# Kernel optimization log

Measured on AMD Instinct MI355X. Metric: run time of the kernel, lower is better.

The kernel has to match this reference:

```python
import jax, jax.numpy as jnp
import numpy as np

N_NODES = 50000
N_EDGES = 1600000
NFEAT = 512
NHID = 64
H1 = 8      # nheads[0]
H2 = 1      # nheads[1]
NCLASS = 16
ALPHA = 0.2  # leaky_relu negative slope


def setup_inputs() -> dict:
    key = jax.random.key(0)
    ks = jax.random.split(key, 6)
    x = jax.random.normal(ks[0], (N_NODES, NFEAT), jnp.float32)
    edge_index = jax.random.randint(ks[1], (2, N_EDGES), 0, N_NODES, jnp.int32)

    def glorot(k, shape):
        fan_in, fan_out = shape[-2], shape[-1]
        std = (2.0 / (fan_in + fan_out)) ** 0.5
        return jax.random.normal(k, shape, jnp.float32) * std

    W1 = glorot(ks[2], (H1, NFEAT, NHID))
    a1 = jax.random.normal(ks[3], (H1, 2 * NHID), jnp.float32) * 0.1
    W2 = glorot(ks[4], (H2, NHID * H1, NCLASS))
    a2 = jax.random.normal(ks[5], (H2, 2 * NCLASS), jnp.float32) * 0.1
    return {"x": x, "edge_index": edge_index, "W1": W1, "a1": a1, "W2": W2, "a2": a2}


def _spgat_head(x, W, a, src, dst, n_nodes, apply_elu):
    # Sparse GAT head (pyGAT SpGraphAttentionLayer, eval mode / no dropout).
    h = x @ W                              # [N, F']
    f = W.shape[1]
    # a . [h_src || h_dst] decomposed into per-node scores (same math, no [E,2F'] concat)
    s_src = h @ a[:f]                      # [N]
    s_dst = h @ a[f:]                      # [N]
    logits = s_src[src] + s_dst[dst]       # [E]
    e = jnp.exp(-jax.nn.leaky_relu(logits, ALPHA))  # edge_e = exp(-leakyrelu(...)) > 0
    rowsum = jax.ops.segment_sum(e, src, num_segments=n_nodes)            # [N]
    agg = jax.ops.segment_sum(e[:, None] * h[dst], src, num_segments=n_nodes)  # [N, F']
    h_prime = agg / rowsum[:, None]
    return jax.nn.elu(h_prime) if apply_elu else h_prime


def reference(x, edge_index, W1, a1, W2, a2):
    src, dst = edge_index[0], edge_index[1]
    n = x.shape[0]
    # Layer 1: H1 heads, concat=True (elu inside each head), concatenated on features
    h = jnp.concatenate(
        [_spgat_head(x, W1[i], a1[i], src, dst, n, True) for i in range(W1.shape[0])],
        axis=1,
    )  # [N, H1*NHID]
    # Layer 2: H2 heads, concat=False, stacked then averaged
    outs = jnp.stack(
        [_spgat_head(h, W2[i], a2[i], src, dst, n, False) for i in range(W2.shape[0])],
        axis=2,
    )  # [N, NCLASS, H2]
    out = jnp.mean(outs, axis=2)
    return jax.nn.log_softmax(jax.nn.elu(out), axis=1)
```

## Files before the change

### kernel.cpp

```cpp
#include <hip/hip_runtime.h>

#define NN 50000
#define NE 1600000
#define NFEAT 512
#define NHID 64
#define H1 8
#define NCLASS 16
#define ALPHA 0.2f

#define BUCKETS 391
#define CAP 6144
#define EPB 4096
#define PASSA_BLKS 391
#define PASSB_BLKS 391
#define PACK_BLKS 1024
#define PACK2_BLKS 32
#define GEMMB 391
#define NROW_PAD 50048

typedef __attribute__((ext_vector_type(8))) short short8;
typedef __attribute__((ext_vector_type(4))) float floatx4;
typedef __attribute__((ext_vector_type(2))) float floatx2;
typedef __attribute__((ext_vector_type(2))) long longx2;

__device__ __forceinline__ float elu_f(float x) { return x > 0.0f ? x : __expf(x) - 1.0f; }
__device__ __forceinline__ float edge_w(float logit) {
    return __expf(-fmaxf(logit, ALPHA * logit));
}
__device__ __forceinline__ ushort f2bf(float f) {
    uint u = __float_as_uint(f);
    return (ushort)((u + 0x7FFFu + ((u >> 16) & 1)) >> 16);
}
__device__ __forceinline__ uint packbf2(float lo, float hi) {
    return (uint)f2bf(lo) | ((uint)f2bf(hi) << 16);
}
__device__ __forceinline__ float bf2f(ushort v) { return __uint_as_float((uint)v << 16); }
__device__ __forceinline__ unsigned char f2fp8(float v) {
    return (unsigned char)(__builtin_amdgcn_cvt_pk_fp8_f32(v, v, 0, false) & 0xFF);
}
__device__ __forceinline__ uint pack4fp8(float a, float b, float c, float d) {
    uint u = __builtin_amdgcn_cvt_pk_fp8_f32(a, b, 0, false);
    return __builtin_amdgcn_cvt_pk_fp8_f32(c, d, u, true);
}

#define GLD16(g, l)                                                              \
    __builtin_amdgcn_global_load_lds(                                            \
        (const __attribute__((address_space(1))) unsigned int*)(g),              \
        (__attribute__((address_space(3))) unsigned int*)(l), 16, 0, 0)

__device__ __forceinline__ int scan256x(int v, int tid, int* wsum, int* tot) {
    int s = v;
#pragma unroll
    for (int o = 1; o < 64; o <<= 1) {
        int u = __shfl_up(s, o);
        if ((tid & 63) >= o) s += u;
    }
    __syncthreads();
    if ((tid & 63) == 63) wsum[tid >> 6] = s;
    __syncthreads();
    int off = 0, t = 0;
#pragma unroll
    for (int i = 0; i < 4; i++) {
        int x = wsum[i];
        if (i < (tid >> 6)) off += x;
        t += x;
    }
    *tot = t;
    return s - v + off;
}

__device__ __forceinline__ int scan512x(int v, int tid, int* wsum, int* tot) {
    int s = v;
#pragma unroll
    for (int o = 1; o < 64; o <<= 1) {
        int u = __shfl_up(s, o);
        if ((tid & 63) >= o) s += u;
    }
    __syncthreads();
    if ((tid & 63) == 63) wsum[tid >> 6] = s;
    __syncthreads();
    int off = 0, t = 0;
#pragma unroll
    for (int i = 0; i < 8; i++) {
        int x = wsum[i];
        if (i < (tid >> 6)) off += x;
        t += x;
    }
    *tot = t;
    return s - v + off;
}

__global__ __launch_bounds__(256) void prep_k(const float* __restrict__ W1,
                                              unsigned char* __restrict__ Wt8,
                                              const float* __restrict__ W2,
                                              ushort* __restrict__ W2tb,
                                              const int* __restrict__ ei,
                                              int* __restrict__ bucket_cnt,
                                              uint* __restrict__ staging) {
    int b = blockIdx.x;
    if (b < PACK_BLKS) {
        int i = b * 256 + threadIdx.x;
        int c = i >> 9, o = i & 511;
        int c6 = o >> 6, qhi = (o >> 4) & 3, kb = (o >> 3) & 1, bb = o & 7;
        int quad = qhi ^ ((c >> 1) & 3);
        int k = c6 * 64 + kb * 32 + quad * 8 + bb;
        Wt8[i] = f2fp8(W1[((c >> 6) * 512 + k) * 64 + (c & 63)]);
        return;
    }
    if (b < PACK_BLKS + PACK2_BLKS) {
        int i = (b - PACK_BLKS) * 256 + threadIdx.x;
        int c = i >> 9, f = i & 511;
        W2tb[i] = f2bf(W2[f * 16 + c]);
        return;
    }
    __shared__ int histA[BUCKETS];
    __shared__ int exclA[BUCKETS];
    __shared__ int baseA[BUCKETS];
    __shared__ int wsumA[4];
    __shared__ uint ebuf[EPB];
    const int blk = b - PACK_BLKS - PACK2_BLKS;
    const int t = threadIdx.x;
    const int e0 = blk * EPB;
    const int cntb = min(EPB, NE - e0);
    for (int i = t; i < BUCKETS; i += 256) histA[i] = 0;
    __syncthreads();
    int br[16]; uint pay[16];
#pragma unroll
    for (int i = 0; i < 16; i++) {
        int e = e0 + i * 256 + t;
        br[i] = -1;
        if (e < NE) {
            int s = ei[e], d = ei[NE + e];
            int bu = s >> 7;
            pay[i] = ((uint)bu << 23) | ((uint)(s & 127) << 16) | (uint)d;
            br[i] = (bu << 12) | atomicAdd(&histA[bu], 1);
        }
    }
    __syncthreads();
    int tot0, tot1;
    int v0 = histA[t];
    int v1 = (t + 256 < BUCKETS) ? histA[t + 256] : 0;
    int p0 = scan256x(v0, t, wsumA, &tot0);
    int p1 = scan256x(v1, t, wsumA, &tot1);
    exclA[t] = p0;
    if (t + 256 < BUCKETS) exclA[t + 256] = p1 + tot0;
    __syncthreads();
    for (int i = t; i < BUCKETS; i += 256) {
        int c = histA[i];
        if (c > 0) baseA[i] = atomicAdd(&bucket_cnt[i], c);
    }
#pragma unroll
    for (int i = 0; i < 16; i++)
        if (br[i] >= 0) ebuf[exclA[br[i] >> 12] + (br[i] & 4095)] = pay[i];
    __syncthreads();
    for (int j = t; j < cntb; j += 256) {
        uint v = ebuf[j];
        int bu = v >> 23;
        int pos = baseA[bu] + (j - exclA[bu]);
        staging[(size_t)bu * CAP + pos] = v;
    }
}

__global__ __launch_bounds__(512) void passb_k(const int* __restrict__ bucket_cnt,
                                               const uint* __restrict__ staging,
                                               ushort* __restrict__ csru,
                                               int* __restrict__ rowptr) {
    __shared__ int hist2w[1024];
    __shared__ int cur2w[1024];
    __shared__ int wbase[1024];
    __shared__ int excl2[128];
    __shared__ int wsum2[8];
    __shared__ int sbs;
    const int tid = threadIdx.x;
    const int b = blockIdx.x;
    const int cnt = bucket_cnt[b];
    const uint* sg = staging + (size_t)b * CAP;
    const int wv = tid >> 6;
    for (int i = tid; i < 2048; i += 512) {
        if (i < 1024) hist2w[i] = 0; else cur2w[i - 1024] = 0;
    }
    if (tid < 64) {
        int c[7]; int s0 = 0;
#pragma unroll
        for (int i = 0; i < 7; i++) {
            int bi = tid * 7 + i;
            c[i] = (bi < BUCKETS) ? bucket_cnt[bi] : 0;
            s0 += c[i];
        }
        int sc = s0;
#pragma unroll
        for (int o = 1; o < 64; o <<= 1) {
            int u = __shfl_up(sc, o);
            if (tid >= o) sc += u;
        }
        int run = sc - s0;
        if (tid == b / 7) {
            int part = run;
            for (int i = 0; i < b % 7; i++) part += c[i];
            sbs = part;
        }
    }
    if (b == 0 && tid == 0) rowptr[NN] = NE;
    __syncthreads();
    const int sbase = sbs;
    for (int e = tid; e < cnt; e += 512)
        atomicAdd(&hist2w[wv * 128 + ((sg[e] >> 16) & 127)], 1);
    __syncthreads();
    int v = 0;
    if (tid < 128) {
        int run = 0;
#pragma unroll
        for (int w = 0; w < 8; w++) {
            wbase[w * 128 + tid] = run;
            run += hist2w[w * 128 + tid];
        }
        v = run;
    }
    int tot;
    int ex = scan512x(v, tid, wsum2, &tot);
    if (tid < 128) {
        excl2[tid] = ex;
        int n = b * 128 + tid;
        if (n < NN) rowptr[n] = sbase + ex;
    }
    __syncthreads();
    for (int e = tid; e < cnt; e += 512) {
        uint u = sg[e];
        int sl = (u >> 16) & 127;
        int pos = excl2[sl] + wbase[wv * 128 + sl] + atomicAdd(&cur2w[wv * 128 + sl], 1);
        csru[sbase + pos] = (ushort)(u & 0xFFFF);
    }
}

__global__ __launch_bounds__(512) void gemm1_k(const float* __restrict__ x,
                                               const unsigned char* __restrict__ Wt8,
                                               const float* __restrict__ a1,
                                               unsigned char* __restrict__ h8,
                                               float* __restrict__ s1s,
                                               float* __restrict__ s1d) {
    __shared__ unsigned char Bs[32768];
    const int tid = threadIdx.x;
    const int gb = blockIdx.x;
    const int row0 = gb * 128;
    const int wv = tid >> 6, lane = tid & 63;
    const int l16 = lane & 15, quad = lane >> 4;
    const int qoff = ((quad ^ ((l16 >> 1) & 3)) << 4);
    const int mA = wv * 16 + (lane >> 2);
    const int offA = (lane & 3) * 16;
    const unsigned char* gB0 = Wt8 + (size_t)(0 * 128 + mA) * 512 + offA;
    const unsigned char* gB1 = Wt8 + (size_t)(1 * 128 + mA) * 512 + offA;
    const unsigned char* gB2 = Wt8 + (size_t)(2 * 128 + mA) * 512 + offA;
    const unsigned char* gB3 = Wt8 + (size_t)(3 * 128 + mA) * 512 + offA;
    const int arow = row0 + wv * 16 + l16;
    const int arowc = min(arow, NN - 1);
    const float* xA = x + (size_t)arowc * 512 + quad * 8;

    floatx4 acc[32];
#pragma unroll
    for (int ct = 0; ct < 32; ct++) acc[ct] = (floatx4){0.f, 0.f, 0.f, 0.f};

    for (int t = 0; t < 8; t++) {
        const int k0 = t * 64;
        GLD16(gB0 + k0, Bs + wv * 1024);
        GLD16(gB1 + k0, Bs + 8192 + wv * 1024);
        GLD16(gB2 + k0, Bs + 16384 + wv * 1024);
        GLD16(gB3 + k0, Bs + 24576 + wv * 1024);
        float4 f0 = *(const float4*)(xA + k0);
        float4 f1 = *(const float4*)(xA + k0 + 4);
        float4 f2 = *(const float4*)(xA + k0 + 32);
        float4 f3 = *(const float4*)(xA + k0 + 36);
        uint u0 = pack4fp8(f0.x, f0.y, f0.z, f0.w);
        uint u1 = pack4fp8(f1.x, f1.y, f1.z, f1.w);
        uint u2 = pack4fp8(f2.x, f2.y, f2.z, f2.w);
        uint u3 = pack4fp8(f3.x, f3.y, f3.z, f3.w);
        long ax = (long)(((unsigned long)u1 << 32) | u0);
        long ay = (long)(((unsigned long)u3 << 32) | u2);
        __syncthreads();
        const unsigned char* bp = Bs + l16 * 64 + qoff;
#pragma unroll
        for (int ct = 0; ct < 32; ct++) {
            longx2 bv = *(const longx2*)(bp + ct * 1024);
            acc[ct] = __builtin_amdgcn_mfma_f32_16x16x32_fp8_fp8(ax, bv.x, acc[ct], 0, 0, 0);
            acc[ct] = __builtin_amdgcn_mfma_f32_16x16x32_fp8_fp8(ay, bv.y, acc[ct], 0, 0, 0);
        }
        __syncthreads();
    }

    const int rbase = row0 + wv * 16 + quad * 4;
#pragma unroll
    for (int hh = 0; hh < 8; hh++) {
        float ss[4] = {0.f, 0.f, 0.f, 0.f}, sd[4] = {0.f, 0.f, 0.f, 0.f};
#pragma unroll
        for (int c4 = 0; c4 < 4; c4++) {
            int ct = hh * 4 + c4;
            int colg = ct * 16 + l16;
            float avs = a1[hh * 128 + c4 * 16 + l16];
            float avd = a1[hh * 128 + 64 + c4 * 16 + l16];
#pragma unroll
            for (int r = 0; r < 4; r++) {
                float v = acc[ct][r];
                ss[r] += v * avs;
                sd[r] += v * avd;
                int row = rbase + r;
                if (row < NN) h8[(size_t)row * 512 + colg] = f2fp8(v);
            }
        }
#pragma unroll
        for (int r = 0; r < 4; r++) {
            float a_ = ss[r], b_ = sd[r];
#pragma unroll
            for (int o = 1; o < 16; o <<= 1) {
                a_ += __shfl_xor(a_, o);
                b_ += __shfl_xor(b_, o);
            }
            int row = rbase + r;
            if (l16 == 0 && row < NN) {
                s1s[row * 8 + hh] = a_;
                s1d[row * 8 + hh] = b_;
            }
        }
    }
}

__global__ __launch_bounds__(256) void agg1f_k(const int n_base,
                                               const int* __restrict__ rowptr,
                                               const ushort* __restrict__ csru,
                                               const float* __restrict__ s1s,
                                               const float* __restrict__ s1d,
                                               const uint2* __restrict__ hb8,
                                               const ushort* __restrict__ W2tb,
                                               const float* __restrict__ a2,
                                               ushort* __restrict__ h2b,
                                               float* __restrict__ s2s,
                                               float* __restrict__ s2d) {
    __shared__ ushort Ash[16 * 512];
    unsigned char* ashb = (unsigned char*)Ash;
    const int tid = threadIdx.x;
    const int wv = tid >> 6, lane = tid & 63;
    const int n0 = n_base + blockIdx.x * 4;
    const int n = n0 + wv;
    const int head8 = lane >> 3;
    const int hb = head8 << 3;
    const int esub = lane & 7;
    const int beg = rowptr[n];
    const int deg = rowptr[n + 1] - beg;
    const float ssrc = s1s[n * 8 + head8];
    floatx2 acc[4] = {};
    float rsum = 0.f;

    const int G = (deg + 7) >> 3;
    const int dm1 = deg - 1;
    if (G > 0) {
        int dA = csru[beg + min(esub, dm1)];
        float tw = s1d[dA * 8 + head8];
        for (int g = 0; g < G; g++) {
            uint2 v[8];
#pragma unroll
            for (int j = 0; j < 8; j++) {
                int dj = __shfl(dA, j);
                v[j] = hb8[(uint)dj * 64 + lane];
            }
            int dAn = csru[beg + min(g * 8 + 8 + esub, dm1)];
            float twn = s1d[dAn * 8 + head8];
            float w = (g * 8 + esub <= dm1) ? edge_w(ssrc + tw) : 0.f;
            rsum += w;
#pragma unroll
            for (int j = 0; j < 8; j++) {
                float wj = __shfl(w, hb + j);
                floatx2 w2 = (floatx2){wj, wj};
                acc[0] += w2 * __builtin_amdgcn_cvt_pk_f32_fp8(v[j].x, false);
                acc[1] += w2 * __builtin_amdgcn_cvt_pk_f32_fp8(v[j].x, true);
                acc[2] += w2 * __builtin_amdgcn_cvt_pk_f32_fp8(v[j].y, false);
                acc[3] += w2 * __builtin_amdgcn_cvt_pk_f32_fp8(v[j].y, true);
            }
            dA = dAn;
            tw = twn;
        }
    }

    rsum += __shfl_xor(rsum, 1);
    rsum += __shfl_xor(rsum, 2);
    rsum += __shfl_xor(rsum, 4);
    float inv = 1.0f / rsum;
    uint4 o;
    o.x = packbf2(elu_f(acc[0][0] * inv), elu_f(acc[0][1] * inv));
    o.y = packbf2(elu_f(acc[1][0] * inv), elu_f(acc[1][1] * inv));
    o.z = packbf2(elu_f(acc[2][0] * inv), elu_f(acc[2][1] * inv));
    o.w = packbf2(elu_f(acc[3][0] * inv), elu_f(acc[3][1] * inv));
    *(uint4*)(ashb + wv * 1024 + ((lane * 16) ^ (wv << 4))) = o;
    __syncthreads();

    if (wv == 0) {
        const int l16 = lane & 15, q = lane >> 4;
        floatx4 c2 = (floatx4){0.f, 0.f, 0.f, 0.f};
#pragma unroll
        for (int s = 0; s < 16; s++) {
            short8 af = *(const short8*)(ashb + l16 * 1024 +
                                         ((s * 64 + q * 16) ^ ((l16 & 7) << 4)));
            short8 bf = *(const short8*)(W2tb + l16 * 512 + s * 32 + q * 8);
            c2 = __builtin_amdgcn_mfma_f32_16x16x32_bf16(af, bf, c2, 0, 0, 0);
        }
        if (q == 0) {
#pragma unroll
            for (int r = 0; r < 4; r++) h2b[(size_t)(n0 + r) * 16 + l16] = f2bf(c2[r]);
        }
#pragma unroll
        for (int r = 0; r < 4; r++) {
            float ssv = c2[r] * a2[l16];
            float sdv = c2[r] * a2[16 + l16];
#pragma unroll
            for (int oo = 1; oo < 16; oo <<= 1) {
                ssv += __shfl_xor(ssv, oo);
                sdv += __shfl_xor(sdv, oo);
            }
            if (lane == 0) { s2s[n0 + r] = ssv; s2d[n0 + r] = sdv; }
        }
    }
}

__global__ __launch_bounds__(256) void agg2_k(const int* __restrict__ rowptr,
                                              const ushort* __restrict__ csru,
                                              const float* __restrict__ s2s,
                                              const float* __restrict__ s2d,
                                              const ushort* __restrict__ h2b,
                                              float* __restrict__ out) {
    const int n = (blockIdx.x * 256 + threadIdx.x) >> 6;
    const int lane = threadIdx.x & 63;
    if (n >= NN) return;
    const int beg = rowptr[n], end = rowptr[n + 1];
    const float sn = s2s[n];
    const int sub = lane >> 4, f = lane & 15;
    float acc = 0.f, rsum = 0.f;
    int e = beg + sub;
    for (; e + 12 < end; e += 16) {
        int d0 = csru[e], d1 = csru[e + 4], d2 = csru[e + 8], d3 = csru[e + 12];
        float t0 = s2d[d0], t1 = s2d[d1], t2 = s2d[d2], t3 = s2d[d3];
        float g0 = bf2f(h2b[(uint)d0 * 16 + f]), g1 = bf2f(h2b[(uint)d1 * 16 + f]);
        float g2 = bf2f(h2b[(uint)d2 * 16 + f]), g3 = bf2f(h2b[(uint)d3 * 16 + f]);
        float w0 = edge_w(sn + t0), w1 = edge_w(sn + t1);
        float w2 = edge_w(sn + t2), w3 = edge_w(sn + t3);
        acc += w0 * g0 + w1 * g1 + w2 * g2 + w3 * g3;
        rsum += w0 + w1 + w2 + w3;
    }
    for (; e < end; e += 4) {
        int d0 = csru[e];
        float w0 = edge_w(sn + s2d[d0]);
        acc += w0 * bf2f(h2b[(uint)d0 * 16 + f]);
        rsum += w0;
    }
    acc += __shfl_down(acc, 32);
    acc += __shfl_down(acc, 16);
    rsum += __shfl_down(rsum, 32);
    rsum += __shfl_down(rsum, 16);
    if (lane < 16) {
        float v = elu_f(acc / rsum);
        float m = v;
#pragma unroll
        for (int o = 8; o > 0; o >>= 1) m = fmaxf(m, __shfl_xor(m, o));
        float ex = __expf(v - m), s = ex;
#pragma unroll
        for (int o = 8; o > 0; o >>= 1) s += __shfl_xor(s, o);
        out[(size_t)n * 16 + f] = v - (__logf(s) + m);
    }
}

extern "C" void kernel_launch(void* const* d_in, const int* in_sizes, int n_in,
                              void* d_out, int out_size, void* d_ws, size_t ws_size,
                              hipStream_t stream) {
    const float* x  = (const float*)d_in[0];
    const int*   ei = (const int*)d_in[1];
    const float* W1 = (const float*)d_in[2];
    const float* a1 = (const float*)d_in[3];
    const float* W2 = (const float*)d_in[4];
    const float* a2 = (const float*)d_in[5];
    float* out = (float*)d_out;

    unsigned char* h8  = (unsigned char*)d_ws;
    unsigned char* Wt8 = h8 + (size_t)NROW_PAD * 512;
    ushort* W2tb  = (ushort*)(Wt8 + 512 * 512);
    float* s1s    = (float*)(W2tb + 8192);
    float* s1d    = s1s + (size_t)NN * H1;
    int* rowptr   = (int*)(s1d + (size_t)NN * H1);
    int* bucket_cnt   = rowptr + 50056;
    int* bucket_start = bucket_cnt + 512;
    ushort* csru  = (ushort*)(bucket_start + 512);
    ushort* h2b   = csru + NE;
    float* s2s    = (float*)(h2b + (size_t)NN * 16);
    float* s2d    = s2s + NN;
    uint* staging = (uint*)(s2d + NN);

    hipMemsetAsync(bucket_cnt, 0, 512 * sizeof(int), stream);

    prep_k<<<PACK_BLKS + PACK2_BLKS + PASSA_BLKS, 256, 0, stream>>>(
        W1, Wt8, W2, W2tb, ei, bucket_cnt, staging);
    passb_k<<<PASSB_BLKS, 512, 0, stream>>>(bucket_cnt, staging, csru, rowptr);
    gemm1_k<<<GEMMB, 512, 0, stream>>>(x, Wt8, a1, h8, s1s, s1d);
    agg1f_k<<<NN / 8, 256, 0, stream>>>(0, rowptr, csru, s1s, s1d,
                                        (const uint2*)h8, W2tb, a2, h2b, s2s, s2d);
    agg1f_k<<<NN / 8, 256, 0, stream>>>(NN / 2, rowptr, csru, s1s, s1d,
                                        (const uint2*)h8, W2tb, a2, h2b, s2s, s2d);
    agg2_k<<<(NN + 3) / 4, 256, 0, stream>>>(rowptr, csru, s2s, s2d, h2b, out);
}
```

Before: 401.6 us.

## Fuse edge bucketing pass into GEMM1 launch and unroll agg2 loop deeper

After: 398.0 us. About the same (-0.9%).

```diff
diff --git a/kernel.cpp b/kernel.cpp
--- a/kernel.cpp
+++ b/kernel.cpp
@@ -48,27 +48,6 @@
         (const __attribute__((address_space(1))) unsigned int*)(g),              \
         (__attribute__((address_space(3))) unsigned int*)(l), 16, 0, 0)
 
-__device__ __forceinline__ int scan256x(int v, int tid, int* wsum, int* tot) {
-    int s = v;
-#pragma unroll
-    for (int o = 1; o < 64; o <<= 1) {
-        int u = __shfl_up(s, o);
-        if ((tid & 63) >= o) s += u;
-    }
-    __syncthreads();
-    if ((tid & 63) == 63) wsum[tid >> 6] = s;
-    __syncthreads();
-    int off = 0, t = 0;
-#pragma unroll
-    for (int i = 0; i < 4; i++) {
-        int x = wsum[i];
-        if (i < (tid >> 6)) off += x;
-        t += x;
-    }
-    *tot = t;
-    return s - v + off;
-}
-
 __device__ __forceinline__ int scan512x(int v, int tid, int* wsum, int* tot) {
     int s = v;
 #pragma unroll
@@ -90,13 +69,10 @@
     return s - v + off;
 }
 
-__global__ __launch_bounds__(256) void prep_k(const float* __restrict__ W1,
-                                              unsigned char* __restrict__ Wt8,
-                                              const float* __restrict__ W2,
-                                              ushort* __restrict__ W2tb,
-                                              const int* __restrict__ ei,
-                                              int* __restrict__ bucket_cnt,
-                                              uint* __restrict__ staging) {
+__global__ __launch_bounds__(256) void prep_w_k(const float* __restrict__ W1,
+                                                unsigned char* __restrict__ Wt8,
+                                                const float* __restrict__ W2,
+                                                ushort* __restrict__ W2tb) {
     int b = blockIdx.x;
     if (b < PACK_BLKS) {
         int i = b * 256 + threadIdx.x;
@@ -107,57 +83,149 @@
         Wt8[i] = f2fp8(W1[((c >> 6) * 512 + k) * 64 + (c & 63)]);
         return;
     }
-    if (b < PACK_BLKS + PACK2_BLKS) {
-        int i = (b - PACK_BLKS) * 256 + threadIdx.x;
-        int c = i >> 9, f = i & 511;
-        W2tb[i] = f2bf(W2[f * 16 + c]);
+    int i = (b - PACK_BLKS) * 256 + threadIdx.x;
+    int c = i >> 9, f = i & 511;
+    W2tb[i] = f2bf(W2[f * 16 + c]);
+}
+
+__global__ __launch_bounds__(512) void passa_gemm1_k(const int* __restrict__ ei,
+                                                     int* __restrict__ bucket_cnt,
+                                                     uint* __restrict__ staging,
+                                                     const float* __restrict__ x,
+                                                     const unsigned char* __restrict__ Wt8,
+                                                     const float* __restrict__ a1,
+                                                     unsigned char* __restrict__ h8,
+                                                     float* __restrict__ s1s,
+                                                     float* __restrict__ s1d) {
+    __shared__ unsigned char shmem[32768];
+    const int tid = threadIdx.x;
+
+    if (blockIdx.x < PASSA_BLKS) {
+        int* histA = (int*)shmem;
+        int* exclA = histA + 400;
+        int* baseA = exclA + 400;
+        int* wsumA = baseA + 400;
+        uint* ebuf = (uint*)(wsumA + 8);
+        const int blk = blockIdx.x;
+        const int e0 = blk * EPB;
+        const int cntb = min(EPB, NE - e0);
+        for (int i = tid; i < BUCKETS; i += 512) histA[i] = 0;
+        __syncthreads();
+        int br[8]; uint pay[8];
+#pragma unroll
+        for (int i = 0; i < 8; i++) {
+            int e = e0 + i * 512 + tid;
+            br[i] = -1;
+            if (e < NE) {
+                int s = ei[e], d = ei[NE + e];
+                int bu = s >> 7;
+                pay[i] = ((uint)bu << 23) | ((uint)(s & 127) << 16) | (uint)d;
+                br[i] = (bu << 12) | atomicAdd(&histA[bu], 1);
+            }
+        }
+        __syncthreads();
+        int v = (tid < BUCKETS) ? histA[tid] : 0;
+        int tot;
+        int ex = scan512x(v, tid, wsumA, &tot);
+        if (tid < BUCKETS) exclA[tid] = ex;
+        __syncthreads();
+        for (int i = tid; i < BUCKETS; i += 512) {
+            int c = histA[i];
+            if (c > 0) baseA[i] = atomicAdd(&bucket_cnt[i], c);
+        }
+#pragma unroll
+        for (int i = 0; i < 8; i++)
+            if (br[i] >= 0) ebuf[exclA[br[i] >> 12] + (br[i] & 4095)] = pay[i];
+        __syncthreads();
+        for (int j = tid; j < cntb; j += 512) {
+            uint u = ebuf[j];
+            int bu = u >> 23;
+            int pos = baseA[bu] + (j - exclA[bu]);
+            staging[(size_t)bu * CAP + pos] = u;
+        }
         return;
     }
-    __shared__ int histA[BUCKETS];
-    __shared__ int exclA[BUCKETS];
-    __shared__ int baseA[BUCKETS];
-    __shared__ int wsumA[4];
-    __shared__ uint ebuf[EPB];
-    const int blk = b - PACK_BLKS - PACK2_BLKS;
-    const int t = threadIdx.x;
-    const int e0 = blk * EPB;
-    const int cntb = min(EPB, NE - e0);
-    for (int i = t; i < BUCKETS; i += 256) histA[i] = 0;
-    __syncthreads();
-    int br[16]; uint pay[16];
-#pragma unroll
-    for (int i = 0; i < 16; i++) {
-        int e = e0 + i * 256 + t;
-        br[i] = -1;
-        if (e < NE) {
-            int s = ei[e], d = ei[NE + e];
-            int bu = s >> 7;
-            pay[i] = ((uint)bu << 23) | ((uint)(s & 127) << 16) | (uint)d;
-            br[i] = (bu << 12) | atomicAdd(&histA[bu], 1);
-        }
-    }
-    __syncthreads();
-    int tot0, tot1;
-    int v0 = histA[t];
-    int v1 = (t + 256 < BUCKETS) ? histA[t + 256] : 0;
-    int p0 = scan256x(v0, t, wsumA, &tot0);
-    int p1 = scan256x(v1, t, wsumA, &tot1);
-    exclA[t] = p0;
-    if (t + 256 < BUCKETS) exclA[t + 256] = p1 + tot0;
-    __syncthreads();
-    for (int i = t; i < BUCKETS; i += 256) {
-        int c = histA[i];
-        if (c > 0) baseA[i] = atomicAdd(&bucket_cnt[i], c);
-    }
-#pragma unroll
-    for (int i = 0; i < 16; i++)
-        if (br[i] >= 0) ebuf[exclA[br[i] >> 12] + (br[i] & 4095)] = pay[i];
-    __syncthreads();
-    for (int j = t; j < cntb; j += 256) {
-        uint v = ebuf[j];
-        int bu = v >> 23;
-        int pos = baseA[bu] + (j - exclA[bu]);
-        staging[(size_t)bu * CAP + pos] = v;
+
+    unsigned char* Bs = shmem;
+    const int gb = blockIdx.x - PASSA_BLKS;
+    const int row0 = gb * 128;
+    const int wv = tid >> 6, lane = tid & 63;
+    const int l16 = lane & 15, quad = lane >> 4;
+    const int qoff = ((quad ^ ((l16 >> 1) & 3)) << 4);
+    const int mA = wv * 16 + (lane >> 2);
+    const int offA = (lane & 3) * 16;
+    const unsigned char* gB0 = Wt8 + (size_t)(0 * 128 + mA) * 512 + offA;
+    const unsigned char* gB1 = Wt8 + (size_t)(1 * 128 + mA) * 512 + offA;
+    const unsigned char* gB2 = Wt8 + (size_t)(2 * 128 + mA) * 512 + offA;
+    const unsigned char* gB3 = Wt8 + (size_t)(3 * 128 + mA) * 512 + offA;
+    const int arow = row0 + wv * 16 + l16;
+    const int arowc = min(arow, NN - 1);
+    const float* xA = x + (size_t)arowc * 512 + quad * 8;
+
+    floatx4 acc[32];
+#pragma unroll
+    for (int ct = 0; ct < 32; ct++) acc[ct] = (floatx4){0.f, 0.f, 0.f, 0.f};
+
+    for (int t = 0; t < 8; t++) {
+        const int k0 = t * 64;
+        GLD16(gB0 + k0, Bs + wv * 1024);
+        GLD16(gB1 + k0, Bs + 8192 + wv * 1024);
+        GLD16(gB2 + k0, Bs + 16384 + wv * 1024);
+        GLD16(gB3 + k0, Bs + 24576 + wv * 1024);
+        float4 f0 = *(const float4*)(xA + k0);
+        float4 f1 = *(const float4*)(xA + k0 + 4);
+        float4 f2 = *(const float4*)(xA + k0 + 32);
+        float4 f3 = *(const float4*)(xA + k0 + 36);
+        uint u0 = pack4fp8(f0.x, f0.y, f0.z, f0.w);
+        uint u1 = pack4fp8(f1.x, f1.y, f1.z, f1.w);
+        uint u2 = pack4fp8(f2.x, f2.y, f2.z, f2.w);
+        uint u3 = pack4fp8(f3.x, f3.y, f3.z, f3.w);
+        long ax = (long)(((unsigned long)u1 << 32) | u0);
+        long ay = (long)(((unsigned long)u3 << 32) | u2);
+        __syncthreads();
+        const unsigned char* bp = Bs + l16 * 64 + qoff;
+#pragma unroll
+        for (int ct = 0; ct < 32; ct++) {
+            longx2 bv = *(const longx2*)(bp + ct * 1024);
+            acc[ct] = __builtin_amdgcn_mfma_f32_16x16x32_fp8_fp8(ax, bv.x, acc[ct], 0, 0, 0);
+            acc[ct] = __builtin_amdgcn_mfma_f32_16x16x32_fp8_fp8(ay, bv.y, acc[ct], 0, 0, 0);
+        }
+        __syncthreads();
+    }
+
+    const int rbase = row0 + wv * 16 + quad * 4;
+#pragma unroll
+    for (int hh = 0; hh < 8; hh++) {
+        float ss[4] = {0.f, 0.f, 0.f, 0.f}, sd[4] = {0.f, 0.f, 0.f, 0.f};
+#pragma unroll
+        for (int c4 = 0; c4 < 4; c4++) {
+            int ct = hh * 4 + c4;
+            int colg = ct * 16 + l16;
+            float avs = a1[hh * 128 + c4 * 16 + l16];
+            float avd = a1[hh * 128 + 64 + c4 * 16 + l16];
+#pragma unroll
+            for (int r = 0; r < 4; r++) {
+                float v = acc[ct][r];
+                ss[r] += v * avs;
+                sd[r] += v * avd;
+                int row = rbase + r;
+                if (row < NN) h8[(size_t)row * 512 + colg] = f2fp8(v);
+            }
+        }
+#pragma unroll
+        for (int r = 0; r < 4; r++) {
+            float a_ = ss[r], b_ = sd[r];
+#pragma unroll
+            for (int o = 1; o < 16; o <<= 1) {
+                a_ += __shfl_xor(a_, o);
+                b_ += __shfl_xor(b_, o);
+            }
+            int row = rbase + r;
+            if (l16 == 0 && row < NN) {
+                s1s[row * 8 + hh] = a_;
+                s1d[row * 8 + hh] = b_;
+            }
+        }
     }
 }
 
@@ -229,96 +297,6 @@
         int sl = (u >> 16) & 127;
         int pos = excl2[sl] + wbase[wv * 128 + sl] + atomicAdd(&cur2w[wv * 128 + sl], 1);
         csru[sbase + pos] = (ushort)(u & 0xFFFF);
-    }
-}
-
-__global__ __launch_bounds__(512) void gemm1_k(const float* __restrict__ x,
-                                               const unsigned char* __restrict__ Wt8,
-                                               const float* __restrict__ a1,
-                                               unsigned char* __restrict__ h8,
-                                               float* __restrict__ s1s,
-                                               float* __restrict__ s1d) {
-    __shared__ unsigned char Bs[32768];
-    const int tid = threadIdx.x;
-    const int gb = blockIdx.x;
-    const int row0 = gb * 128;
-    const int wv = tid >> 6, lane = tid & 63;
-    const int l16 = lane & 15, quad = lane >> 4;
-    const int qoff = ((quad ^ ((l16 >> 1) & 3)) << 4);
-    const int mA = wv * 16 + (lane >> 2);
-    const int offA = (lane & 3) * 16;
-    const unsigned char* gB0 = Wt8 + (size_t)(0 * 128 + mA) * 512 + offA;
-    const unsigned char* gB1 = Wt8 + (size_t)(1 * 128 + mA) * 512 + offA;
-    const unsigned char* gB2 = Wt8 + (size_t)(2 * 128 + mA) * 512 + offA;
-    const unsigned char* gB3 = Wt8 + (size_t)(3 * 128 + mA) * 512 + offA;
-    const int arow = row0 + wv * 16 + l16;
-    const int arowc = min(arow, NN - 1);
-    const float* xA = x + (size_t)arowc * 512 + quad * 8;
-
-    floatx4 acc[32];
-#pragma unroll
-    for (int ct = 0; ct < 32; ct++) acc[ct] = (floatx4){0.f, 0.f, 0.f, 0.f};
-
-    for (int t = 0; t < 8; t++) {
-        const int k0 = t * 64;
-        GLD16(gB0 + k0, Bs + wv * 1024);
-        GLD16(gB1 + k0, Bs + 8192 + wv * 1024);
-        GLD16(gB2 + k0, Bs + 16384 + wv * 1024);
-        GLD16(gB3 + k0, Bs + 24576 + wv * 1024);
-        float4 f0 = *(const float4*)(xA + k0);
-        float4 f1 = *(const float4*)(xA + k0 + 4);
-        float4 f2 = *(const float4*)(xA + k0 + 32);
-        float4 f3 = *(const float4*)(xA + k0 + 36);
-        uint u0 = pack4fp8(f0.x, f0.y, f0.z, f0.w);
-        uint u1 = pack4fp8(f1.x, f1.y, f1.z, f1.w);
-        uint u2 = pack4fp8(f2.x, f2.y, f2.z, f2.w);
-        uint u3 = pack4fp8(f3.x, f3.y, f3.z, f3.w);
-        long ax = (long)(((unsigned long)u1 << 32) | u0);
-        long ay = (long)(((unsigned long)u3 << 32) | u2);
-        __syncthreads();
-        const unsigned char* bp = Bs + l16 * 64 + qoff;
-#pragma unroll
-        for (int ct = 0; ct < 32; ct++) {
-            longx2 bv = *(const longx2*)(bp + ct * 1024);
-            acc[ct] = __builtin_amdgcn_mfma_f32_16x16x32_fp8_fp8(ax, bv.x, acc[ct], 0, 0, 0);
-            acc[ct] = __builtin_amdgcn_mfma_f32_16x16x32_fp8_fp8(ay, bv.y, acc[ct], 0, 0, 0);
-        }
-        __syncthreads();
-    }
-
-    const int rbase = row0 + wv * 16 + quad * 4;
-#pragma unroll
-    for (int hh = 0; hh < 8; hh++) {
-        float ss[4] = {0.f, 0.f, 0.f, 0.f}, sd[4] = {0.f, 0.f, 0.f, 0.f};
-#pragma unroll
-        for (int c4 = 0; c4 < 4; c4++) {
-            int ct = hh * 4 + c4;
-            int colg = ct * 16 + l16;
-            float avs = a1[hh * 128 + c4 * 16 + l16];
-            float avd = a1[hh * 128 + 64 + c4 * 16 + l16];
-#pragma unroll
-            for (int r = 0; r < 4; r++) {
-                float v = acc[ct][r];
-                ss[r] += v * avs;
-                sd[r] += v * avd;
-                int row = rbase + r;
-                if (row < NN) h8[(size_t)row * 512 + colg] = f2fp8(v);
-            }
-        }
-#pragma unroll
-        for (int r = 0; r < 4; r++) {
-            float a_ = ss[r], b_ = sd[r];
-#pragma unroll
-            for (int o = 1; o < 16; o <<= 1) {
-                a_ += __shfl_xor(a_, o);
-                b_ += __shfl_xor(b_, o);
-            }
-            int row = rbase + r;
-            if (l16 == 0 && row < NN) {
-                s1s[row * 8 + hh] = a_;
-                s1d[row * 8 + hh] = b_;
-            }
-        }
     }
 }
 
@@ -432,6 +410,23 @@
     const int sub = lane >> 4, f = lane & 15;
     float acc = 0.f, rsum = 0.f;
     int e = beg + sub;
+    for (; e + 28 < end; e += 32) {
+        int d0 = csru[e], d1 = csru[e + 4], d2 = csru[e + 8], d3 = csru[e + 12];
+        int d4 = csru[e + 16], d5 = csru[e + 20], d6 = csru[e + 24], d7 = csru[e + 28];
+        float t0 = s2d[d0], t1 = s2d[d1], t2 = s2d[d2], t3 = s2d[d3];
+        float t4 = s2d[d4], t5 = s2d[d5], t6 = s2d[d6], t7 = s2d[d7];
+        float g0 = bf2f(h2b[(uint)d0 * 16 + f]), g1 = bf2f(h2b[(uint)d1 * 16 + f]);
+        float g2 = bf2f(h2b[(uint)d2 * 16 + f]), g3 = bf2f(h2b[(uint)d3 * 16 + f]);
+        float g4 = bf2f(h2b[(uint)d4 * 16 + f]), g5 = bf2f(h2b[(uint)d5 * 16 + f]);
+        float g6 = bf2f(h2b[(uint)d6 * 16 + f]), g7 = bf2f(h2b[(uint)d7 * 16 + f]);
+        float w0 = edge_w(sn + t0), w1 = edge_w(sn + t1);
+        float w2 = edge_w(sn + t2), w3 = edge_w(sn + t3);
+        float w4 = edge_w(sn + t4), w5 = edge_w(sn + t5);
+        float w6 = edge_w(sn + t6), w7 = edge_w(sn + t7);
+        acc += w0 * g0 + w1 * g1 + w2 * g2 + w3 * g3;
+        acc += w4 * g4 + w5 * g5 + w6 * g6 + w7 * g7;
+        rsum += w0 + w1 + w2 + w3 + w4 + w5 + w6 + w7;
+    }
     for (; e + 12 < end; e += 16) {
         int d0 = csru[e], d1 = csru[e + 4], d2 = csru[e + 8], d3 = csru[e + 12];
         float t0 = s2d[d0], t1 = s2d[d1], t2 = s2d[d2], t3 = s2d[d3];
@@ -491,10 +486,10 @@
 
     hipMemsetAsync(bucket_cnt, 0, 512 * sizeof(int), stream);
 
-    prep_k<<<PACK_BLKS + PACK2_BLKS + PASSA_BLKS, 256, 0, stream>>>(
-        W1, Wt8, W2, W2tb, ei, bucket_cnt, staging);
+    prep_w_k<<<PACK_BLKS + PACK2_BLKS, 256, 0, stream>>>(W1, Wt8, W2, W2tb);
+    passa_gemm1_k<<<PASSA_BLKS + GEMMB, 512, 0, stream>>>(ei, bucket_cnt, staging,
+                                                          x, Wt8, a1, h8, s1s, s1d);
     passb_k<<<PASSB_BLKS, 512, 0, stream>>>(bucket_cnt, staging, csru, rowptr);
-    gemm1_k<<<GEMMB, 512, 0, stream>>>(x, Wt8, a1, h8, s1s, s1d);
     agg1f_k<<<NN / 8, 256, 0, stream>>>(0, rowptr, csru, s1s, s1d,
                                         (const uint2*)h8, W2tb, a2, h2b, s2s, s2d);
     agg1f_k<<<NN / 8, 256, 0, stream>>>(NN / 2, rowptr, csru, s1s, s1d,
```
